# Kernel tuning notes

Hardware: AMD Instinct MI355X
Metric: run time of the kernel (lower is better)

## Reference

```python
import jax, jax.numpy as jnp
import numpy as np

EMBED_DIM = 1024
NUM_HEADS = 16
HEAD_DIM = EMBED_DIM // NUM_HEADS  # 64
MLP_DIM = 4096
EPS = 1e-5  # torch LayerNorm default


def layer_norm(x, gamma, beta):
    mu = jnp.mean(x, axis=-1, keepdims=True)
    var = jnp.mean(jnp.square(x - mu), axis=-1, keepdims=True)
    return (x - mu) * jax.lax.rsqrt(var + EPS) * gamma + beta


def setup_inputs() -> dict:
    key = jax.random.key(0)
    ks = jax.random.split(key, 12)
    s = 0.02
    x = jax.random.normal(ks[0], (2, 2048, EMBED_DIM), dtype=jnp.float32)
    # per-head qkv projections (Linear(embed_dim, 3*head_dim, bias=False)), stacked over heads
    w_qkv = s * jax.random.normal(ks[1], (NUM_HEADS, EMBED_DIM, 3 * HEAD_DIM), dtype=jnp.float32)
    # per-head output proj (Linear(head_dim, head_dim), with bias)
    w_hproj = s * jax.random.normal(ks[2], (NUM_HEADS, HEAD_DIM, HEAD_DIM), dtype=jnp.float32)
    b_hproj = jnp.zeros((NUM_HEADS, HEAD_DIM), dtype=jnp.float32)
    # MHA final proj (Linear(num_heads*head_dim, embed_dim))
    w_out = s * jax.random.normal(ks[3], (NUM_HEADS * HEAD_DIM, EMBED_DIM), dtype=jnp.float32)
    b_out = jnp.zeros((EMBED_DIM,), dtype=jnp.float32)
    # MLP
    w_fc1 = s * jax.random.normal(ks[4], (EMBED_DIM, MLP_DIM), dtype=jnp.float32)
    b_fc1 = jnp.zeros((MLP_DIM,), dtype=jnp.float32)
    w_fc2 = s * jax.random.normal(ks[5], (MLP_DIM, EMBED_DIM), dtype=jnp.float32)
    b_fc2 = jnp.zeros((EMBED_DIM,), dtype=jnp.float32)
    # layer norms
    g1 = jnp.ones((EMBED_DIM,), dtype=jnp.float32)
    be1 = jnp.zeros((EMBED_DIM,), dtype=jnp.float32)
    g2 = jnp.ones((EMBED_DIM,), dtype=jnp.float32)
    be2 = jnp.zeros((EMBED_DIM,), dtype=jnp.float32)
    return dict(x=x, w_qkv=w_qkv, w_hproj=w_hproj, b_hproj=b_hproj,
                w_out=w_out, b_out=b_out, w_fc1=w_fc1, b_fc1=b_fc1,
                w_fc2=w_fc2, b_fc2=b_fc2, g1=g1, be1=be1, g2=g2, be2=be2)


def reference(x, w_qkv, w_hproj, b_hproj, w_out, b_out,
              w_fc1, b_fc1, w_fc2, b_fc2, g1, be1, g2, be2):
    B, S, D = x.shape
    scale = HEAD_DIM ** (-0.5)

    # ---- MSA branch (pre-norm, dropouts are identity at eval) ----
    xn = layer_norm(x, g1, be1)
    qkv = jnp.einsum('bsd,hdf->bhsf', xn, w_qkv)  # [B,H,S,3*hd]
    q, k, v = jnp.split(qkv, 3, axis=-1)           # each [B,H,S,hd]
    attn = jax.nn.softmax(jnp.einsum('bhsd,bhtd->bhst', q, k) * scale, axis=-1)
    o = jnp.einsum('bhst,bhtd->bhsd', attn, v)     # [B,H,S,hd]
    o = jnp.einsum('bhsd,hde->bhse', o, w_hproj) + b_hproj[None, :, None, :]
    # concat heads along last dim (head 0 first), then final proj
    o = o.transpose(0, 2, 1, 3).reshape(B, S, NUM_HEADS * HEAD_DIM)
    o = o @ w_out + b_out
    x = x + o

    # ---- MLP branch ----
    xn = layer_norm(x, g2, be2)
    h = jax.nn.gelu(xn @ w_fc1 + b_fc1, approximate=False)
    x = x + (h @ w_fc2 + b_fc2)
    return x
```

## Files before the change

kernel.cpp:

```cpp
#include <hip/hip_runtime.h>
#include <hip/hip_bf16.h>
#include <math.h>

#define DEV __device__ __forceinline__

typedef float f32x4 __attribute__((ext_vector_type(4)));
typedef short bf16x8 __attribute__((ext_vector_type(8)));

DEV unsigned short f2bf(float f) {
  union { float f; unsigned int u; } c; c.f = f;
  return (unsigned short)((c.u + 0x7FFF + ((c.u >> 16) & 1)) >> 16);
}
DEV float bf2f(unsigned short u) {
  union { unsigned int u; float f; } c; c.u = ((unsigned int)u) << 16;
  return c.f;
}

#define ASYNC_LD16(gp, lp)                                                     \
  __builtin_amdgcn_global_load_lds(                                            \
      (const __attribute__((address_space(1))) void*)(gp),                     \
      (__attribute__((address_space(3))) void*)(lp), 16, 0, 0)

__global__ void trans_f32_bf16(const float* __restrict__ in, unsigned short* __restrict__ out,
                               int R, int C, long inBatch, long outBatch) {
  __shared__ float tile[64][65];
  int ct = blockIdx.x, rt = blockIdx.y, z = blockIdx.z;
  const float* src = in + (long)z * inBatch + (long)rt * 64 * C + ct * 64;
  unsigned short* dst = out + (long)z * outBatch + (long)ct * 64 * R + rt * 64;
  int t = threadIdx.x, c = t & 63, r0 = t >> 6;
#pragma unroll
  for (int i = 0; i < 16; i++) {
    int r = i * 4 + r0;
    tile[r][c] = src[(long)r * C + c];
  }
  __syncthreads();
#pragma unroll
  for (int i = 0; i < 16; i++) {
    int r = i * 4 + r0;
    dst[(long)r * R + c] = f2bf(tile[c][r]);
  }
}

__global__ void combine_wout(const float* __restrict__ w_hproj, const float* __restrict__ w_out,
                             unsigned short* __restrict__ wcombt) {
  int hd = blockIdx.x;
  int h = hd >> 6, d = hd & 63;
  for (int i = 0; i < 4; i++) {
    int e = threadIdx.x + i * 256;
    float acc = 0.f;
    for (int dp = 0; dp < 64; dp++)
      acc += w_hproj[(h * 64 + d) * 64 + dp] * w_out[(h * 64 + dp) * 1024 + e];
    wcombt[(long)e * 1024 + hd] = f2bf(acc);
  }
}

__global__ void combine_bias(const float* __restrict__ b_hproj, const float* __restrict__ w_out,
                             const float* __restrict__ b_out, float* __restrict__ bcomb) {
  __shared__ float part[8][32];
  int e = blockIdx.x * 32 + (threadIdx.x & 31);
  int ks = threadIdx.x >> 5;
  float acc = 0.f;
  for (int k = ks * 128; k < ks * 128 + 128; k++) acc += b_hproj[k] * w_out[(long)k * 1024 + e];
  part[ks][threadIdx.x & 31] = acc;
  __syncthreads();
  if (threadIdx.x < 32) {
    float s = b_out[e];
#pragma unroll
    for (int i = 0; i < 8; i++) s += part[i][threadIdx.x];
    bcomb[e] = s;
  }
}

__global__ void transpose_v(const unsigned short* __restrict__ in, unsigned short* __restrict__ out) {
  __shared__ unsigned short tile[64][65];
  int st = blockIdx.x, bh = blockIdx.y;
  const unsigned short* src = in + (long)bh * 131072 + (long)st * 64 * 64;
  unsigned short* dst = out + (long)bh * 131072 + (long)st * 64;
  int t = threadIdx.x, c = t & 63, r0 = t >> 6;
#pragma unroll
  for (int i = 0; i < 16; i++) tile[i * 4 + r0][c] = src[(i * 4 + r0) * 64 + c];
  __syncthreads();
  int kb = c >> 4, g = kb >> 1, sub = kb & 1, hi2 = (c >> 2) & 3, jj = c & 3;
  int pos = g * 32 + hi2 * 8 + sub * 4 + jj;
#pragma unroll
  for (int i = 0; i < 16; i++) {
    int d = i * 4 + r0;
    dst[(long)d * 2048 + pos] = tile[c][d];
  }
}

__launch_bounds__(256)
__global__ void ln_kernel(const float* __restrict__ x, const float* __restrict__ g,
                          const float* __restrict__ b, unsigned short* __restrict__ out) {
  int row = blockIdx.x, t = threadIdx.x;
  float4 v = ((const float4*)(x + (long)row * 1024))[t];
  float s = v.x + v.y + v.z + v.w;
  float s2 = v.x * v.x + v.y * v.y + v.z * v.z + v.w * v.w;
  for (int o = 32; o; o >>= 1) { s += __shfl_down(s, o); s2 += __shfl_down(s2, o); }
  __shared__ float red[8];
  int w = t >> 6, l = t & 63;
  if (l == 0) { red[w] = s; red[w + 4] = s2; }
  __syncthreads();
  s = red[0] + red[1] + red[2] + red[3];
  s2 = red[4] + red[5] + red[6] + red[7];
  float mu = s * (1.f / 1024.f);
  float var = s2 * (1.f / 1024.f) - mu * mu;
  float rs = rsqrtf(var + 1e-5f);
  float4 gv = ((const float4*)g)[t];
  float4 bv = ((const float4*)b)[t];
  ushort4 o4;
  o4.x = f2bf((v.x - mu) * rs * gv.x + bv.x);
  o4.y = f2bf((v.y - mu) * rs * gv.y + bv.y);
  o4.z = f2bf((v.z - mu) * rs * gv.z + bv.z);
  o4.w = f2bf((v.w - mu) * rs * gv.w + bv.w);
  ((ushort4*)(out + (long)row * 1024))[t] = o4;
}

template <int ACCUM>
__launch_bounds__(256)
__global__ void reduce_add(const unsigned short* __restrict__ p0,
                           const unsigned short* __restrict__ p1,
                           const float* __restrict__ bias, const float* __restrict__ resid,
                           float* __restrict__ out) {
  int i = blockIdx.x * 256 + threadIdx.x;
  float4 b = ((const float4*)bias)[i & 255];
  ushort4 a0 = ((const ushort4*)p0)[i];
  ushort4 a1 = ((const ushort4*)p1)[i];
  float4 r = ACCUM ? ((const float4*)out)[i] : ((const float4*)resid)[i];
  float4 o;
  o.x = r.x + b.x + bf2f(a0.x) + bf2f(a1.x);
  o.y = r.y + b.y + bf2f(a0.y) + bf2f(a1.y);
  o.z = r.z + b.z + bf2f(a0.z) + bf2f(a1.z);
  o.w = r.w + b.w + bf2f(a0.w) + bf2f(a1.w);
  ((float4*)out)[i] = o;
}

#define EPI_QKV 0
#define EPI_GELU 2
#define EPI_PARTIAL 3

template <int EPI>
__launch_bounds__(256)
__global__ void gemm_bt(const unsigned short* __restrict__ A, const unsigned short* __restrict__ Bt,
                        int N, int K, const float* __restrict__ bias,
                        unsigned short* __restrict__ outb,
                        unsigned short* __restrict__ qb, unsigned short* __restrict__ kb,
                        unsigned short* __restrict__ vb,
                        unsigned short* __restrict__ pp0, unsigned short* __restrict__ pp1) {
  __shared__ alignas(16) unsigned short lds_a[2][128 * 64];
  __shared__ alignas(16) unsigned short lds_b[2][128 * 64];
  int gx = gridDim.x, nwg = gx * gridDim.y;
  int orig = blockIdx.y * gx + blockIdx.x;
  int cpx = nwg >> 3;
  int wg = (orig & 7) * cpx + (orig >> 3);
  int bm = wg % gx, bn = wg / gx;

  int nk = (K >> 6) / gridDim.z;
  int kbase = blockIdx.z * nk * 64;

  int t = threadIdx.x, w = t >> 6, l = t & 63;
  int wm = w >> 1, wn = w & 1;
  int lr = l & 15, lh = l >> 4;

  f32x4 acc[4][4];
  const f32x4 z4 = {0.f, 0.f, 0.f, 0.f};
#pragma unroll
  for (int m = 0; m < 4; m++)
#pragma unroll
    for (int n = 0; n < 4; n++) acc[m][n] = z4;

#define GSTAGE(buf, kt)                                                        \
  do {                                                                         \
    _Pragma("unroll")                                                          \
    for (int i = 0; i < 4; i++) {                                              \
      int e = i * 2048 + w * 512 + l * 8;                                      \
      int row = e >> 6, col = e & 63;                                          \
      ASYNC_LD16(A + (long)(bm * 128 + row) * K + kbase + (kt) * 64 + col,     \
                 lds_a[buf] + i * 2048 + w * 512);                             \
      ASYNC_LD16(Bt + (long)(bn * 128 + row) * K + kbase + (kt) * 64 + col,    \
                 lds_b[buf] + i * 2048 + w * 512);                             \
    }                                                                          \
  } while (0)

  GSTAGE(0, 0);
  asm volatile("s_waitcnt vmcnt(0)" ::: "memory");
  asm volatile("s_barrier" ::: "memory");

  for (int kt = 0; kt < nk; ++kt) {
    int cur = kt & 1;
    if (kt + 1 < nk) GSTAGE(cur ^ 1, kt + 1);
#pragma unroll
    for (int kc = 0; kc < 2; kc++) {
      bf16x8 af[4], bfr[4];
#pragma unroll
      for (int m = 0; m < 4; m++)
        af[m] = *(const bf16x8*)&lds_a[cur][(wm * 64 + m * 16 + lr) * 64 + kc * 32 + lh * 8];
#pragma unroll
      for (int n = 0; n < 4; n++)
        bfr[n] = *(const bf16x8*)&lds_b[cur][(wn * 64 + n * 16 + lr) * 64 + kc * 32 + lh * 8];
      __builtin_amdgcn_s_setprio(1);
#pragma unroll
      for (int m = 0; m < 4; m++)
#pragma unroll
        for (int n = 0; n < 4; n++)
          acc[m][n] = __builtin_amdgcn_mfma_f32_16x16x32_bf16(af[m], bfr[n], acc[m][n], 0, 0, 0);
      __builtin_amdgcn_s_setprio(0);
    }
    if (kt + 1 < nk) {
      asm volatile("s_waitcnt vmcnt(0)" ::: "memory");
      asm volatile("s_barrier" ::: "memory");
    }
  }
#undef GSTAGE

#pragma unroll
  for (int m = 0; m < 4; m++) {
#pragma unroll
    for (int n = 0; n < 4; n++) {
      int c = bn * 128 + wn * 64 + n * 16 + lr;
#pragma unroll
      for (int j = 0; j < 4; j++) {
        int r = bm * 128 + wm * 64 + m * 16 + lh * 4 + j;
        float val = acc[m][n][j];
        if (EPI == EPI_QKV) {
          int h = c / 192, f = c - h * 192;
          int part = f >> 6, d = f & 63;
          int b = r >> 11, s = r & 2047;
          long idx = ((long)(b * 16 + h) * 2048 + s) * 64 + d;
          if (part == 0) qb[idx] = f2bf(val * 0.18033688011112042f);
          else if (part == 1) kb[idx] = f2bf(val);
          else vb[idx] = f2bf(val);
        } else if (EPI == EPI_GELU) {
          float u = val + bias[c];
          float z2 = u * (0.7978845608f + 0.0356774081f * u * u) * 2.885390082f;
          float e2 = exp2f(z2);
          float th = 1.f - 2.f / (e2 + 1.f);
          outb[(long)r * N + c] = f2bf(0.5f * u * (1.f + th));
        } else {
          unsigned short* pd = blockIdx.z ? pp1 : pp0;
          pd[(long)r * N + c] = f2bf(val);
        }
      }
    }
  }
}

__launch_bounds__(256)
__global__ void attn_kernel(const unsigned short* __restrict__ Qg,
                            const unsigned short* __restrict__ Kg,
                            const unsigned short* __restrict__ Vt,
                            unsigned short* __restrict__ Og) {
  __shared__ alignas(16) unsigned short k_lds[2][64 * 64];
  __shared__ alignas(16) unsigned short v_lds[2][64 * 64];
  int orig = blockIdx.y * 32 + blockIdx.x;
  int wg = (orig & 7) * 128 + (orig >> 3);
  int qt = wg & 31, bh = wg >> 5;

  int t = threadIdx.x, w = t >> 6, l = t & 63, lr = l & 15, hi = l >> 4;
  const unsigned short* Qh = Qg + (long)bh * 131072;
  const char* Kh = (const char*)(Kg + (long)bh * 131072);
  const char* Vh = (const char*)(Vt + (long)bh * 131072);

  int qrow = qt * 64 + w * 16 + lr;
  bf16x8 qf0 = *(const bf16x8*)(Qh + (long)qrow * 64 + hi * 8);
  bf16x8 qf1 = *(const bf16x8*)(Qh + (long)qrow * 64 + 32 + hi * 8);
  asm volatile("" :: "v"(qf0), "v"(qf1));

  const f32x4 z4 = {0.f, 0.f, 0.f, 0.f};
  f32x4 accO[4];
#pragma unroll
  for (int j = 0; j < 4; j++) accO[j] = z4;
  float m_q = -1e30f, lsum = 0.f;

#define STAGE(b, kt)                                                           \
  do {                                                                         \
    _Pragma("unroll")                                                          \
    for (int i = 0; i < 2; i++) {                                              \
      int o = (t + i * 256) * 16;                                              \
      int row = o >> 7;                                                        \
      int colb = (o & 127) ^ ((row & 7) << 4);                                 \
      ASYNC_LD16(Kh + (long)((kt) * 64 + row) * 128 + colb,                    \
                 (char*)k_lds[b] + (w * 64 + i * 256) * 16);                   \
      ASYNC_LD16(Vh + (long)row * 4096 + (kt) * 128 + colb,                    \
                 (char*)v_lds[b] + (w * 64 + i * 256) * 16);                   \
    }                                                                          \
  } while (0)

  STAGE(0, 0);

  for (int kt = 0; kt < 32; ++kt) {
    int cur = kt & 1;
    if (kt < 31) {
      STAGE(cur ^ 1, kt + 1);
      asm volatile("s_waitcnt vmcnt(4)" ::: "memory");
    } else {
      asm volatile("s_waitcnt vmcnt(0)" ::: "memory");
    }
    __builtin_amdgcn_s_barrier();

    f32x4 sacc[4];
#pragma unroll
    for (int kbk = 0; kbk < 4; kbk++) sacc[kbk] = z4;
    __builtin_amdgcn_s_setprio(1);
#pragma unroll
    for (int kbk = 0; kbk < 4; kbk++) {
      int krow = kbk * 16 + lr;
      int sw = (krow & 7) << 4;
      const char* kbase = (const char*)k_lds[cur] + krow * 128;
      bf16x8 kf0 = *(const bf16x8*)(kbase + ((hi * 16) ^ sw));
      bf16x8 kf1 = *(const bf16x8*)(kbase + ((64 + hi * 16) ^ sw));
      sacc[kbk] = __builtin_amdgcn_mfma_f32_16x16x32_bf16(kf0, qf0, sacc[kbk], 0, 0, 0);
      sacc[kbk] = __builtin_amdgcn_mfma_f32_16x16x32_bf16(kf1, qf1, sacc[kbk], 0, 0, 0);
    }
    __builtin_amdgcn_s_setprio(0);

    float mx = -1e30f;
#pragma unroll
    for (int kbk = 0; kbk < 4; kbk++)
#pragma unroll
      for (int r = 0; r < 4; r++) mx = fmaxf(mx, sacc[kbk][r]);
    mx = fmaxf(mx, __shfl_xor(mx, 16));
    mx = fmaxf(mx, __shfl_xor(mx, 32));
    if (!__all(mx <= m_q + 8.f)) {
      float mnew = fmaxf(m_q, mx);
      float fac = exp2f(m_q - mnew);
      m_q = mnew;
      lsum *= fac;
      float fj[4];
#pragma unroll
      for (int j = 0; j < 4; j++) fj[j] = __shfl(fac, ((l >> 4) << 2) | j);
#pragma unroll
      for (int db = 0; db < 4; db++)
#pragma unroll
        for (int j = 0; j < 4; j++) accO[db][j] *= fj[j];
    }
    float rs = 0.f;
#pragma unroll
    for (int kbk = 0; kbk < 4; kbk++)
#pragma unroll
      for (int r = 0; r < 4; r++) {
        float p = exp2f(sacc[kbk][r] - m_q);
        sacc[kbk][r] = p;
        rs += p;
      }
    rs += __shfl_xor(rs, 16);
    rs += __shfl_xor(rs, 32);
    lsum += rs;

    bf16x8 pa0, pa1;
#pragma unroll
    for (int r = 0; r < 4; r++) {
      pa0[r] = (short)f2bf(sacc[0][r]);
      pa0[r + 4] = (short)f2bf(sacc[1][r]);
      pa1[r] = (short)f2bf(sacc[2][r]);
      pa1[r + 4] = (short)f2bf(sacc[3][r]);
    }

    __builtin_amdgcn_s_setprio(1);
#pragma unroll
    for (int g = 0; g < 2; g++) {
      bf16x8 pf = g ? pa1 : pa0;
#pragma unroll
      for (int db = 0; db < 4; db++) {
        int d = db * 16 + lr;
        int sw = (d & 7) << 4;
        bf16x8 vf = *(const bf16x8*)((const char*)v_lds[cur] + d * 128 + ((g * 64 + hi * 16) ^ sw));
        accO[db] = __builtin_amdgcn_mfma_f32_16x16x32_bf16(pf, vf, accO[db], 0, 0, 0);
      }
    }
    __builtin_amdgcn_s_setprio(0);

    if (kt < 31) {
      asm volatile("s_waitcnt lgkmcnt(0)" ::: "memory");
      __builtin_amdgcn_s_barrier();
    }
  }
#undef STAGE

  float linv[4];
#pragma unroll
  for (int j = 0; j < 4; j++) linv[j] = 1.f / __shfl(lsum, ((l >> 4) << 2) | j);

  int b = bh >> 4, h = bh & 15;
#pragma unroll
  for (int db = 0; db < 4; db++)
#pragma unroll
    for (int j = 0; j < 4; j++) {
      int s = qt * 64 + w * 16 + hi * 4 + j;
      Og[((long)(b * 2048 + s)) * 1024 + h * 64 + db * 16 + lr] = f2bf(accO[db][j] * linv[j]);
    }
}

extern "C" void kernel_launch(void* const* d_in, const int* in_sizes, int n_in,
                              void* d_out, int out_size, void* d_ws, size_t ws_size,
                              hipStream_t stream) {
  const float* x = (const float*)d_in[0];
  const float* w_qkv = (const float*)d_in[1];
  const float* w_hproj = (const float*)d_in[2];
  const float* b_hproj = (const float*)d_in[3];
  const float* w_out = (const float*)d_in[4];
  const float* b_out = (const float*)d_in[5];
  const float* w_fc1 = (const float*)d_in[6];
  const float* b_fc1 = (const float*)d_in[7];
  const float* w_fc2 = (const float*)d_in[8];
  const float* b_fc2 = (const float*)d_in[9];
  const float* g1 = (const float*)d_in[10];
  const float* be1 = (const float*)d_in[11];
  const float* g2 = (const float*)d_in[12];
  const float* be2 = (const float*)d_in[13];
  float* out = (float*)d_out;

  char* ws = (char*)d_ws;
  unsigned short* wqkvt = (unsigned short*)(ws + 0);
  unsigned short* wfc1t = (unsigned short*)(ws + 6291456);
  unsigned short* wfc2t = (unsigned short*)(ws + 14680064);
  unsigned short* wcombt = (unsigned short*)(ws + 23068672);
  float* bcomb = (float*)(ws + 25165824);
  unsigned short* xn = (unsigned short*)(ws + 25169920);
  unsigned short* qb = (unsigned short*)(ws + 33558528);
  unsigned short* kb = (unsigned short*)(ws + 41947136);
  unsigned short* vb = (unsigned short*)(ws + 50335744);
  unsigned short* attn_o = (unsigned short*)(ws + 58724352);
  unsigned short* h1 = qb;
  unsigned short* vt = xn;

  trans_f32_bf16<<<dim3(3, 16, 16), 256, 0, stream>>>(w_qkv, wqkvt, 1024, 192,
                                                      196608L, 196608L);
  trans_f32_bf16<<<dim3(64, 16, 1), 256, 0, stream>>>(w_fc1, wfc1t, 1024, 4096, 0, 0);
  trans_f32_bf16<<<dim3(16, 64, 1), 256, 0, stream>>>(w_fc2, wfc2t, 4096, 1024, 0, 0);
  combine_wout<<<1024, 256, 0, stream>>>(w_hproj, w_out, wcombt);
  combine_bias<<<32, 256, 0, stream>>>(b_hproj, w_out, b_out, bcomb);

  ln_kernel<<<4096, 256, 0, stream>>>(x, g1, be1, xn);
  gemm_bt<EPI_QKV><<<dim3(32, 24, 1), 256, 0, stream>>>(xn, wqkvt, 3072, 1024,
      nullptr, nullptr, qb, kb, vb, nullptr, nullptr);
  transpose_v<<<dim3(32, 32), 256, 0, stream>>>(vb, vt);
  attn_kernel<<<dim3(32, 32), 256, 0, stream>>>(qb, kb, vt, attn_o);
  gemm_bt<EPI_PARTIAL><<<dim3(32, 8, 2), 256, 0, stream>>>(attn_o, wcombt, 1024, 1024,
      nullptr, nullptr, nullptr, nullptr, nullptr, qb, kb);
  reduce_add<0><<<4096, 256, 0, stream>>>(qb, kb, bcomb, x, out);

  ln_kernel<<<4096, 256, 0, stream>>>(out, g2, be2, xn);
  gemm_bt<EPI_GELU><<<dim3(32, 32, 1), 256, 0, stream>>>(xn, wfc1t, 4096, 1024,
      b_fc1, h1, nullptr, nullptr, nullptr, nullptr, nullptr);
  gemm_bt<EPI_PARTIAL><<<dim3(32, 8, 2), 256, 0, stream>>>(h1, wfc2t, 1024, 4096,
      nullptr, nullptr, nullptr, nullptr, nullptr, xn, wfc1t);
  reduce_add<1><<<4096, 256, 0, stream>>>(xn, wfc1t, b_fc2, nullptr, out);
}
```

Baseline: 362.9 us.

## Enlarge GEMM tiles to 256-wide with 8 waves and XOR-swizzled LDS

Replaces the 128x128, 4-wave GEMM with a templated kernel using 256-column (and 256- or 128-row) tiles, 512 threads and 8 waves. LDS rows are now XOR-swizzled to avoid bank conflicts on fragment reads. Split-K handles uneven splits, and reduce_add is generalized to up to four partials, though still called with two. Larger tiles raise operand reuse per byte loaded but cut the number of workgroups, use more LDS and registers, and may lower occupancy.

Measured after the change: 322.2 us. 1.13x faster.

```diff
diff --git a/kernel.cpp b/kernel.cpp
--- a/kernel.cpp
+++ b/kernel.cpp
@@ -116,22 +116,32 @@
   ((ushort4*)(out + (long)row * 1024))[t] = o4;
 }
 
-template <int ACCUM>
+template <int NP, int ACCUM>
 __launch_bounds__(256)
 __global__ void reduce_add(const unsigned short* __restrict__ p0,
                            const unsigned short* __restrict__ p1,
+                           const unsigned short* __restrict__ p2,
+                           const unsigned short* __restrict__ p3,
                            const float* __restrict__ bias, const float* __restrict__ resid,
                            float* __restrict__ out) {
   int i = blockIdx.x * 256 + threadIdx.x;
   float4 b = ((const float4*)bias)[i & 255];
+  float4 r = ACCUM ? ((const float4*)out)[i] : ((const float4*)resid)[i];
+  float4 o;
   ushort4 a0 = ((const ushort4*)p0)[i];
   ushort4 a1 = ((const ushort4*)p1)[i];
-  float4 r = ACCUM ? ((const float4*)out)[i] : ((const float4*)resid)[i];
-  float4 o;
   o.x = r.x + b.x + bf2f(a0.x) + bf2f(a1.x);
   o.y = r.y + b.y + bf2f(a0.y) + bf2f(a1.y);
   o.z = r.z + b.z + bf2f(a0.z) + bf2f(a1.z);
   o.w = r.w + b.w + bf2f(a0.w) + bf2f(a1.w);
+  if (NP > 2) {
+    ushort4 a2 = ((const ushort4*)p2)[i];
+    o.x += bf2f(a2.x); o.y += bf2f(a2.y); o.z += bf2f(a2.z); o.w += bf2f(a2.w);
+  }
+  if (NP > 3) {
+    ushort4 a3 = ((const ushort4*)p3)[i];
+    o.x += bf2f(a3.x); o.y += bf2f(a3.y); o.z += bf2f(a3.z); o.w += bf2f(a3.w);
+  }
   ((float4*)out)[i] = o;
 }
 
@@ -139,46 +149,56 @@
 #define EPI_GELU 2
 #define EPI_PARTIAL 3
 
-template <int EPI>
-__launch_bounds__(256)
-__global__ void gemm_bt(const unsigned short* __restrict__ A, const unsigned short* __restrict__ Bt,
+template <int EPI, int BM>
+__launch_bounds__(512, 2)
+__global__ void gemm256(const unsigned short* __restrict__ A, const unsigned short* __restrict__ Bt,
                         int N, int K, const float* __restrict__ bias,
                         unsigned short* __restrict__ outb,
                         unsigned short* __restrict__ qb, unsigned short* __restrict__ kb,
                         unsigned short* __restrict__ vb,
                         unsigned short* __restrict__ pp0, unsigned short* __restrict__ pp1) {
-  __shared__ alignas(16) unsigned short lds_a[2][128 * 64];
-  __shared__ alignas(16) unsigned short lds_b[2][128 * 64];
+  constexpr int MR = BM / 32;
+  __shared__ alignas(16) unsigned short lds_a[2][BM * 64];
+  __shared__ alignas(16) unsigned short lds_b[2][256 * 64];
   int gx = gridDim.x, nwg = gx * gridDim.y;
   int orig = blockIdx.y * gx + blockIdx.x;
   int cpx = nwg >> 3;
   int wg = (orig & 7) * cpx + (orig >> 3);
   int bm = wg % gx, bn = wg / gx;
 
-  int nk = (K >> 6) / gridDim.z;
-  int kbase = blockIdx.z * nk * 64;
+  int tt = K >> 6, Z = gridDim.z, z = blockIdx.z;
+  int bq = tt / Z, rem = tt - bq * Z;
+  int nk = bq + (z < rem ? 1 : 0);
+  int kt0 = z * bq + (z < rem ? z : rem);
 
   int t = threadIdx.x, w = t >> 6, l = t & 63;
-  int wm = w >> 1, wn = w & 1;
-  int lr = l & 15, lh = l >> 4;
-
-  f32x4 acc[4][4];
+  int wm = w >> 2, wn = w & 3;
+  int lr = l & 15, hi = l >> 4;
+
+  f32x4 acc[MR][4];
   const f32x4 z4 = {0.f, 0.f, 0.f, 0.f};
 #pragma unroll
-  for (int m = 0; m < 4; m++)
+  for (int m = 0; m < MR; m++)
 #pragma unroll
     for (int n = 0; n < 4; n++) acc[m][n] = z4;
 
 #define GSTAGE(buf, kt)                                                        \
   do {                                                                         \
     _Pragma("unroll")                                                          \
-    for (int i = 0; i < 4; i++) {                                              \
-      int e = i * 2048 + w * 512 + l * 8;                                      \
-      int row = e >> 6, col = e & 63;                                          \
-      ASYNC_LD16(A + (long)(bm * 128 + row) * K + kbase + (kt) * 64 + col,     \
-                 lds_a[buf] + i * 2048 + w * 512);                             \
-      ASYNC_LD16(Bt + (long)(bn * 128 + row) * K + kbase + (kt) * 64 + col,    \
-                 lds_b[buf] + i * 2048 + w * 512);                             \
+    for (int i = 0; i < BM / 64; i++) {                   \
+      int ch = i * 512 + t;                                                    \
+      int row = ch >> 3, cs = ch & 7;                                          \
+      int csz = cs ^ (row & 7);                                                \
+      ASYNC_LD16(A + (long)(bm * BM + row) * K + (kt0 + (kt)) * 64 + csz * 8,  \
+                 lds_a[buf] + (size_t)ch * 8);                                 \
+    }                                                                          \
+    _Pragma("unroll")                                                          \
+    for (int i = 0; i < 4; i++) {                        \
+      int ch = i * 512 + t;                                                    \
+      int row = ch >> 3, cs = ch & 7;                                          \
+      int csz = cs ^ (row & 7);                                                \
+      ASYNC_LD16(Bt + (long)(bn * 256 + row) * K + (kt0 + (kt)) * 64 + csz * 8,\
+                 lds_b[buf] + (size_t)ch * 8);                                 \
     }                                                                          \
   } while (0)
 
@@ -191,16 +211,22 @@
     if (kt + 1 < nk) GSTAGE(cur ^ 1, kt + 1);
 #pragma unroll
     for (int kc = 0; kc < 2; kc++) {
-      bf16x8 af[4], bfr[4];
-#pragma unroll
-      for (int m = 0; m < 4; m++)
-        af[m] = *(const bf16x8*)&lds_a[cur][(wm * 64 + m * 16 + lr) * 64 + kc * 32 + lh * 8];
-#pragma unroll
-      for (int n = 0; n < 4; n++)
-        bfr[n] = *(const bf16x8*)&lds_b[cur][(wn * 64 + n * 16 + lr) * 64 + kc * 32 + lh * 8];
+      bf16x8 af[MR], bfr[4];
+#pragma unroll
+      for (int m = 0; m < MR; m++) {
+        int row = wm * (BM / 2) + m * 16 + lr;
+        af[m] = *(const bf16x8*)((const char*)lds_a[cur] + row * 128 +
+                                 ((((kc << 2) | hi) ^ (row & 7)) << 4));
+      }
+#pragma unroll
+      for (int n = 0; n < 4; n++) {
+        int row = wn * 64 + n * 16 + lr;
+        bfr[n] = *(const bf16x8*)((const char*)lds_b[cur] + row * 128 +
+                                  ((((kc << 2) | hi) ^ (row & 7)) << 4));
+      }
       __builtin_amdgcn_s_setprio(1);
 #pragma unroll
-      for (int m = 0; m < 4; m++)
+      for (int m = 0; m < MR; m++)
 #pragma unroll
         for (int n = 0; n < 4; n++)
           acc[m][n] = __builtin_amdgcn_mfma_f32_16x16x32_bf16(af[m], bfr[n], acc[m][n], 0, 0, 0);
@@ -214,13 +240,13 @@
 #undef GSTAGE
 
 #pragma unroll
-  for (int m = 0; m < 4; m++) {
+  for (int m = 0; m < MR; m++) {
 #pragma unroll
     for (int n = 0; n < 4; n++) {
-      int c = bn * 128 + wn * 64 + n * 16 + lr;
+      int c = bn * 256 + wn * 64 + n * 16 + lr;
 #pragma unroll
       for (int j = 0; j < 4; j++) {
-        int r = bm * 128 + wm * 64 + m * 16 + lh * 4 + j;
+        int r = bm * BM + wm * (BM / 2) + m * 16 + hi * 4 + j;
         float val = acc[m][n][j];
         if (EPI == EPI_QKV) {
           int h = c / 192, f = c - h * 192;
@@ -237,7 +263,7 @@
           float th = 1.f - 2.f / (e2 + 1.f);
           outb[(long)r * N + c] = f2bf(0.5f * u * (1.f + th));
         } else {
-          unsigned short* pd = blockIdx.z ? pp1 : pp0;
+          unsigned short* pd = (z == 0) ? pp0 : pp1;
           pd[(long)r * N + c] = f2bf(val);
         }
       }
@@ -423,6 +449,8 @@
   unsigned short* attn_o = (unsigned short*)(ws + 58724352);
   unsigned short* h1 = qb;
   unsigned short* vt = xn;
+  unsigned short* f2p0 = wfc1t;
+  unsigned short* f2p1 = xn;
 
   trans_f32_bf16<<<dim3(3, 16, 16), 256, 0, stream>>>(w_qkv, wqkvt, 1024, 192,
                                                       196608L, 196608L);
@@ -432,18 +460,18 @@
   combine_bias<<<32, 256, 0, stream>>>(b_hproj, w_out, b_out, bcomb);
 
   ln_kernel<<<4096, 256, 0, stream>>>(x, g1, be1, xn);
-  gemm_bt<EPI_QKV><<<dim3(32, 24, 1), 256, 0, stream>>>(xn, wqkvt, 3072, 1024,
+  gemm256<EPI_QKV, 256><<<dim3(16, 12, 1), 512, 0, stream>>>(xn, wqkvt, 3072, 1024,
       nullptr, nullptr, qb, kb, vb, nullptr, nullptr);
   transpose_v<<<dim3(32, 32), 256, 0, stream>>>(vb, vt);
   attn_kernel<<<dim3(32, 32), 256, 0, stream>>>(qb, kb, vt, attn_o);
-  gemm_bt<EPI_PARTIAL><<<dim3(32, 8, 2), 256, 0, stream>>>(attn_o, wcombt, 1024, 1024,
+  gemm256<EPI_PARTIAL, 128><<<dim3(32, 4, 2), 512, 0, stream>>>(attn_o, wcombt, 1024, 1024,
       nullptr, nullptr, nullptr, nullptr, nullptr, qb, kb);
-  reduce_add<0><<<4096, 256, 0, stream>>>(qb, kb, bcomb, x, out);
+  reduce_add<2, 0><<<4096, 256, 0, stream>>>(qb, kb, nullptr, nullptr, bcomb, x, out);
 
   ln_kernel<<<4096, 256, 0, stream>>>(out, g2, be2, xn);
-  gemm_bt<EPI_GELU><<<dim3(32, 32, 1), 256, 0, stream>>>(xn, wfc1t, 4096, 1024,
+  gemm256<EPI_GELU, 256><<<dim3(16, 16, 1), 512, 0, stream>>>(xn, wfc1t, 4096, 1024,
       b_fc1, h1, nullptr, nullptr, nullptr, nullptr, nullptr);
-  gemm_bt<EPI_PARTIAL><<<dim3(32, 8, 2), 256, 0, stream>>>(h1, wfc2t, 1024, 4096,
-      nullptr, nullptr, nullptr, nullptr, nullptr, xn, wfc1t);
-  reduce_add<1><<<4096, 256, 0, stream>>>(xn, wfc1t, b_fc2, nullptr, out);
-}
+  gemm256<EPI_PARTIAL, 128><<<dim3(32, 4, 2), 512, 0, stream>>>(h1, wfc2t, 1024, 4096,
+      nullptr, nullptr, nullptr, nullptr, nullptr, f2p0, f2p1);
+  reduce_add<2, 1><<<4096, 256, 0, stream>>>(f2p0, f2p1, nullptr, nullptr, b_fc2, nullptr, out);
+}
```
